# Performance work log

Measured on AMD Instinct MI355X. Metric: run time of the kernel, lower is better.

Reference implementation:

```python
import jax, jax.numpy as jnp
import numpy as np

N_NODES = 50000
N_EDGES = 800000
D = 128
L = 2

def mobius_add(x, y, c):
    xy = jnp.sum(x * y, axis=-1, keepdims=True)
    xx = jnp.sum(x * x, axis=-1, keepdims=True)
    yy = jnp.sum(y * y, axis=-1, keepdims=True)
    num = (1 + 2 * c * xy + c * yy) * x + (1 - c * xx) * y
    den = 1 + 2 * c * xy + c * c * xx * yy
    return num / den

def exp_map(x, v, c):
    vn = jnp.linalg.norm(v, axis=-1, keepdims=True)
    sc = jnp.sqrt(c)
    second = jnp.tanh(sc * vn / 2) * v / (sc * vn)
    return mobius_add(x, second, c)

def log_map(x, y, c):
    a = mobius_add(-x, y, c)
    an = jnp.linalg.norm(a, axis=-1, keepdims=True)
    sc = jnp.sqrt(c)
    return 2 / sc * jnp.arctanh(sc * an) * a / an

def l2norm(x, eps=1e-12):
    n = jnp.linalg.norm(x, axis=-1, keepdims=True)
    return x / jnp.maximum(n, eps)

def mean_agg(h, src, dst, n):
    # DGL update_all(copy_u('h','m'), mean('m','neigh')): mean over incoming edges
    s = jax.ops.segment_sum(h[src], dst, num_segments=n)  # [N, D]
    deg = jax.ops.segment_sum(jnp.ones((src.shape[0], 1), h.dtype), dst, num_segments=n)
    return s / jnp.maximum(deg, 1.0)

def setup_inputs() -> dict:
    key = jax.random.key(0)
    ks = jax.random.split(key, 12)
    w_scale = 1.0 / np.sqrt(D)
    return {
        'src': jax.random.randint(ks[0], (N_EDGES,), 0, N_NODES, dtype=jnp.int32),
        'dst': jax.random.randint(ks[1], (N_EDGES,), 0, N_NODES, dtype=jnp.int32),
        'e_emb': jax.random.normal(ks[2], (N_NODES, D), jnp.float32),
        # hyperbolic embeddings must lie well inside the Poincare ball
        'b_emb': jax.random.normal(ks[3], (N_NODES, D), jnp.float32) * 0.004,
        's_emb': jax.random.normal(ks[4], (N_NODES, D), jnp.float32),
        'e_W': jax.random.normal(ks[5], (L, D, D), jnp.float32) * w_scale,
        'e_b': jax.random.normal(ks[6], (L, D), jnp.float32) * 0.01,
        'b_W': jax.random.normal(ks[7], (L, D, D), jnp.float32) * w_scale,
        'b_b': jax.random.normal(ks[8], (L, D), jnp.float32) * 0.01,
        's_W': jax.random.normal(ks[9], (L, D, D), jnp.float32) * w_scale,
        's_b': jax.random.normal(ks[10], (L, D), jnp.float32) * 0.01,
        'b_curv': jnp.ones((1,), jnp.float32),
        's_curv': jnp.ones((1,), jnp.float32),
    }

def reference(src, dst, e_emb, b_emb, s_emb, e_W, e_b, b_W, b_b, s_W, s_b, b_curv, s_curv):
    n = e_emb.shape[0]
    bc = b_curv[0]
    sc = s_curv[0]
    for l in range(L):
        # euclidean: linear -> mean-aggregate -> LeakyReLU(0.2)
        e_h = e_emb @ e_W[l].T + e_b[l]
        e_new = mean_agg(e_h, src, dst, n)
        # hyperbolic: log-map to tangent at origin -> linear -> mean -> exp-map
        origin = jnp.zeros((1, D), b_emb.dtype)
        tang = log_map(origin, b_emb, bc)
        b_h = tang @ b_W[l].T + b_b[l]
        b_agg = mean_agg(b_h, src, dst, n)
        b_new = exp_map(origin, b_agg, bc)
        # spherical: normalize -> linear -> normalize -> mean -> normalize
        s_h = l2norm(s_emb)
        s_h = l2norm(s_h @ s_W[l].T + s_b[l])
        s_new = l2norm(mean_agg(s_h, src, dst, n))
        e_emb = jax.nn.leaky_relu(e_new, 0.2)
        b_emb = b_new
        s_emb = s_new
    return jnp.concatenate([e_emb, b_emb, s_emb], axis=1)  # [N, 3*D]
```

## Files before the change

### kernel.cpp

```cpp
#include <hip/hip_runtime.h>
#include <hip/hip_bf16.h>

#define NN 50000
#define NE 800000
#define DD 128

typedef unsigned int u32;
typedef __attribute__((ext_vector_type(8))) short short8;
typedef __attribute__((ext_vector_type(4))) float f32x4;
typedef __attribute__((ext_vector_type(2))) float f32x2;
typedef __attribute__((ext_vector_type(4))) u32 u32x4;

__device__ __forceinline__ u32 f2bf2(float a, float b){
  union { __hip_bfloat162 h; u32 u; } cv;
  cv.h = __float22bfloat162_rn(make_float2(a, b));
  return cv.u;
}
__device__ __forceinline__ f32x2 up2(u32 v){
  f32x2 r;
  r.x = __uint_as_float(v << 16);
  r.y = __uint_as_float(v & 0xffff0000u);
  return r;
}

struct InitArgs { const float* W[6]; u32* out; const int* dst; int* cnt; int* rank; };
__global__ __launch_bounds__(256) void k_init(InitArgs ia){
  const int bx = blockIdx.x;
  if (bx < 48){
    int tid = bx*256 + threadIdx.x;
    int mat = tid >> 11, rem = tid & 2047;
    int frag = rem >> 6, lane = rem & 63;
    int ct = frag >> 2, ks = frag & 3, rr = lane & 15, quad = lane >> 4;
    const float* p = ia.W[mat] + (ct*16 + rr)*128 + ks*32 + quad*8;
    float4 f0 = *(const float4*)p;
    float4 f1 = *(const float4*)(p + 4);
    u32x4 q;
    q.x = f2bf2(f0.x, f0.y); q.y = f2bf2(f0.z, f0.w);
    q.z = f2bf2(f1.x, f1.y); q.w = f2bf2(f1.z, f1.w);
    *(u32x4*)(ia.out + (size_t)tid*4) = q;
  } else {
    int i = (bx - 48)*256 + threadIdx.x;
    if (i < NE){
      int d = ia.dst[i];
      ia.rank[i] = atomicAdd(&ia.cnt[d], 1);
    }
  }
}

__global__ __launch_bounds__(256) void k_alloc(const int* __restrict__ cnt,
                                               int* __restrict__ row_beg,
                                               int* __restrict__ gcount){
  int i = blockIdx.x*256 + threadIdx.x;
  int lane = threadIdx.x & 63;
  int pc = (i < NN) ? ((cnt[i] + 1) & ~1) : 0;
  int incl = pc;
  #pragma unroll
  for (int off = 1; off < 64; off <<= 1){
    int u = __shfl_up(incl, off, 64);
    if (lane >= off) incl += u;
  }
  int wtot = __shfl(incl, 63, 64);
  int base = 0;
  if (lane == 0) base = atomicAdd(gcount, wtot);
  base = __shfl(base, 0, 64);
  int excl = base + incl - pc;
  if (i < NN) row_beg[i] = excl;
}

struct MainArgs {
  const float* A[3];
  const float* Bias[3];
  const u32* Wf;
  u32* H;
  const float* curv;
  const int* src;
  const int* dst;
  const int* rank;
  const int* row_beg;
  int* esrc;
};

#define GEMM_BLKS 471

__global__ __launch_bounds__(256,3) void k_main(MainArgs ma){
  const int bx = blockIdx.x;
  if (bx >= GEMM_BLKS){
    int i = (bx - GEMM_BLKS)*256 + threadIdx.x;
    if (i < NE){
      int d = ma.dst[i];
      ma.esrc[ma.row_beg[d] + ma.rank[i]] = (ma.src[i] + 1) * 192;
    }
    return;
  }
  const int m  = bx / 157;
  const int gx = bx % 157;
  const float* __restrict__ A    = ma.A[m];
  const float* __restrict__ Bias = ma.Bias[m];
  u32* __restrict__ H = ma.H;
  const int t = threadIdx.x;
  const int lane = t & 63;
  const int rr = lane & 15, quad = lane >> 4;

  __shared__ u32 Wlds[8192];
  {
    const u32x4* wsrc = (const u32x4*)(ma.Wf + (size_t)m*8192);
    #pragma unroll
    for (int it = 0; it < 8; ++it){
      int idx = it*256 + t;
      *(u32x4*)&Wlds[idx*4] = wsrc[idx];
    }
  }
  __syncthreads();

  float sc = 1.f;
  if (m == 1) sc = sqrtf(*ma.curv);

  const int nw = 157*4;
  for (int g = gx*4 + (t >> 6); g < 3125; g += nw){
    const float* ap = A + (size_t)(g*16 + rr)*DD + quad*8;
    float4 c[8];
    #pragma unroll
    for (int ks = 0; ks < 4; ++ks){
      c[2*ks]   = *(const float4*)(ap + ks*32);
      c[2*ks+1] = *(const float4*)(ap + ks*32 + 4);
    }
    if (m != 0){
      float p = 0.f;
      #pragma unroll
      for (int i = 0; i < 8; ++i)
        p += c[i].x*c[i].x + c[i].y*c[i].y + c[i].z*c[i].z + c[i].w*c[i].w;
      p += __shfl_xor(p, 16, 64);
      p += __shfl_xor(p, 32, 64);
      float nrm = sqrtf(p);
      float sca;
      if (m == 1){
        float x = sc * nrm;
        sca = (nrm > 1e-30f) ? (logf((1.f + x)/(1.f - x)) / (sc * nrm)) : 2.f;
      } else {
        sca = 1.f / fmaxf(nrm, 1e-12f);
      }
      #pragma unroll
      for (int i = 0; i < 8; ++i){ c[i].x*=sca; c[i].y*=sca; c[i].z*=sca; c[i].w*=sca; }
    }
    f32x4 acc[8];
    #pragma unroll
    for (int ct = 0; ct < 8; ++ct){ f32x4 z = {0.f,0.f,0.f,0.f}; acc[ct] = z; }
    #pragma unroll
    for (int ks = 0; ks < 4; ++ks){
      u32x4 bq;
      bq.x = f2bf2(c[2*ks].x,   c[2*ks].y);
      bq.y = f2bf2(c[2*ks].z,   c[2*ks].w);
      bq.z = f2bf2(c[2*ks+1].x, c[2*ks+1].y);
      bq.w = f2bf2(c[2*ks+1].z, c[2*ks+1].w);
      short8 bf = __builtin_bit_cast(short8, bq);
      #pragma unroll
      for (int ct = 0; ct < 8; ++ct){
        short8 wf = *(const short8*)&Wlds[((ct*4 + ks)*64 + lane)*4];
        acc[ct] = __builtin_amdgcn_mfma_f32_16x16x32_bf16(wf, bf, acc[ct], 0, 0, 0);
      }
    }
    #pragma unroll
    for (int ct = 0; ct < 8; ++ct){
      float4 bv = *(const float4*)(Bias + ct*16 + quad*4);
      acc[ct].x += bv.x; acc[ct].y += bv.y; acc[ct].z += bv.z; acc[ct].w += bv.w;
    }
    if (m == 2){
      float p = 0.f;
      #pragma unroll
      for (int ct = 0; ct < 8; ++ct)
        p += acc[ct].x*acc[ct].x + acc[ct].y*acc[ct].y + acc[ct].z*acc[ct].z + acc[ct].w*acc[ct].w;
      p += __shfl_xor(p, 16, 64);
      p += __shfl_xor(p, 32, 64);
      float inv = 1.f / fmaxf(sqrtf(p), 1e-12f);
      #pragma unroll
      for (int ct = 0; ct < 8; ++ct){ acc[ct].x*=inv; acc[ct].y*=inv; acc[ct].z*=inv; acc[ct].w*=inv; }
    }
    u32* hp = H + (size_t)(g*16 + rr + 1)*192 + m*64 + quad*2;
    #pragma unroll
    for (int ct = 0; ct < 8; ++ct){
      uint2 pk;
      pk.x = f2bf2(acc[ct].x, acc[ct].y);
      pk.y = f2bf2(acc[ct].z, acc[ct].w);
      *(uint2*)(hp + ct*8) = pk;
    }
  }
}

struct FusedArgs {
  const u32* H0;
  u32* H1;
  const int* row_beg;
  const int* cnt;
  const int* esrc;
  const u32* Wf;
  const float* Bias[3];
};

#define NSTR 388

__global__ __launch_bounds__(256,4) void k_fused(FusedArgs fa){
  const int t = threadIdx.x;
  const int w = t >> 6;
  const int lane = t & 63;
  const int half = lane >> 5, hl = lane & 31;
  const int rr = lane & 15, quad = lane >> 4;
  const int nbase = blockIdx.x * 16;

  __shared__ float S[16*NSTR];

  for (int i = 0; i < 4; ++i){
    const int nb = w*4 + i;
    const int node = nbase + nb;
    const int deg = fa.cnt[node];
    const int e0 = fa.row_beg[node];
    const int e1 = e0 + ((deg + 1) & ~1);
    const int* __restrict__ esrc = fa.esrc;
    const u32* __restrict__ Hf = fa.H0 + hl*2;

    f32x2 z2 = {0.f, 0.f};
    f32x2 a0[2] = {z2, z2};
    f32x2 a1[2] = {z2, z2};
    f32x2 a2[2] = {z2, z2};

    for (int base = e0; base < e1; base += 64){
      int nn = e1 - base; if (nn > 64) nn = 64;
      int sv = esrc[min(base + lane, e1 - 1)];
      int np = nn >> 1;
      int p = 0;
      for (; p + 4 <= np; p += 4){
        uint2 q[4][3];
        #pragma unroll
        for (int u = 0; u < 4; ++u){
          int soff = __shfl(sv, 2*(p + u) + half, 64);
          const u32* hp = Hf + soff;
          q[u][0] = *(const uint2*)hp;
          q[u][1] = *(const uint2*)(hp + 64);
          q[u][2] = *(const uint2*)(hp + 128);
        }
        #pragma unroll
        for (int u = 0; u < 4; ++u){
          a0[0] += up2(q[u][0].x); a0[1] += up2(q[u][0].y);
          a1[0] += up2(q[u][1].x); a1[1] += up2(q[u][1].y);
          a2[0] += up2(q[u][2].x); a2[1] += up2(q[u][2].y);
        }
      }
      for (; p < np; ++p){
        int soff = __shfl(sv, 2*p + half, 64);
        const u32* hp = Hf + soff;
        uint2 q0 = *(const uint2*)hp;
        uint2 q1 = *(const uint2*)(hp + 64);
        uint2 q2 = *(const uint2*)(hp + 128);
        a0[0] += up2(q0.x); a0[1] += up2(q0.y);
        a1[0] += up2(q1.x); a1[1] += up2(q1.y);
        a2[0] += up2(q2.x); a2[1] += up2(q2.y);
      }
    }

    #pragma unroll
    for (int j = 0; j < 2; ++j){
      a0[j].x += __shfl_xor(a0[j].x, 32, 64); a0[j].y += __shfl_xor(a0[j].y, 32, 64);
      a1[j].x += __shfl_xor(a1[j].x, 32, 64); a1[j].y += __shfl_xor(a1[j].y, 32, 64);
      a2[j].x += __shfl_xor(a2[j].x, 32, 64); a2[j].y += __shfl_xor(a2[j].y, 32, 64);
    }
    float inv = 1.f / (float)max(deg, 1);
    #pragma unroll
    for (int j = 0; j < 2; ++j){ a0[j] *= inv; a1[j] *= inv; a2[j] *= inv; }

    float p2 = a2[0].x*a2[0].x + a2[0].y*a2[0].y + a2[1].x*a2[1].x + a2[1].y*a2[1].y;
    #pragma unroll
    for (int off = 1; off < 32; off <<= 1) p2 += __shfl_xor(p2, off, 64);
    float s2 = 1.f / fmaxf(sqrtf(p2), 1e-12f);

    float* sp = &S[nb*NSTR];
    if (half == 0){
      f32x4 v0 = { a0[0].x > 0.f ? a0[0].x : 0.2f*a0[0].x,
                   a0[0].y > 0.f ? a0[0].y : 0.2f*a0[0].y,
                   a0[1].x > 0.f ? a0[1].x : 0.2f*a0[1].x,
                   a0[1].y > 0.f ? a0[1].y : 0.2f*a0[1].y };
      *(f32x4*)(sp + hl*4) = v0;
      f32x4 v1 = { a1[0].x, a1[0].y, a1[1].x, a1[1].y };
      *(f32x4*)(sp + 128 + hl*4) = v1;
    } else {
      f32x4 v2 = { a2[0].x*s2, a2[0].y*s2, a2[1].x*s2, a2[1].y*s2 };
      *(f32x4*)(sp + 256 + hl*4) = v2;
    }
  }
  __syncthreads();

  if (w < 3){
    const int m = w;
    short8 bf[4];
    const float* sp = &S[rr*NSTR + m*128];
    #pragma unroll
    for (int ks = 0; ks < 4; ++ks){
      f32x4 lo = *(const f32x4*)(sp + ks*32 + quad*8);
      f32x4 hi = *(const f32x4*)(sp + ks*32 + quad*8 + 4);
      u32x4 bq;
      bq.x = f2bf2(lo.x, lo.y); bq.y = f2bf2(lo.z, lo.w);
      bq.z = f2bf2(hi.x, hi.y); bq.w = f2bf2(hi.z, hi.w);
      bf[ks] = __builtin_bit_cast(short8, bq);
    }
    const u32* __restrict__ wbase = fa.Wf + (size_t)m*8192;
    const float* __restrict__ Bias = fa.Bias[m];
    f32x4 acc[8];
    #pragma unroll
    for (int ct = 0; ct < 8; ++ct){ f32x4 z = {0.f,0.f,0.f,0.f}; acc[ct] = z; }
    #pragma unroll
    for (int ct = 0; ct < 8; ++ct){
      short8 wfr[4];
      #pragma unroll
      for (int ks = 0; ks < 4; ++ks)
        wfr[ks] = *(const short8*)(wbase + ((ct*4 + ks)*64 + lane)*4);
      #pragma unroll
      for (int ks = 0; ks < 4; ++ks)
        acc[ct] = __builtin_amdgcn_mfma_f32_16x16x32_bf16(wfr[ks], bf[ks], acc[ct], 0, 0, 0);
    }
    #pragma unroll
    for (int ct = 0; ct < 8; ++ct){
      float4 bv = *(const float4*)(Bias + ct*16 + quad*4);
      acc[ct].x += bv.x; acc[ct].y += bv.y; acc[ct].z += bv.z; acc[ct].w += bv.w;
    }
    if (m == 2){
      float p = 0.f;
      #pragma unroll
      for (int ct = 0; ct < 8; ++ct)
        p += acc[ct].x*acc[ct].x + acc[ct].y*acc[ct].y + acc[ct].z*acc[ct].z + acc[ct].w*acc[ct].w;
      p += __shfl_xor(p, 16, 64);
      p += __shfl_xor(p, 32, 64);
      float nv = 1.f / fmaxf(sqrtf(p), 1e-12f);
      #pragma unroll
      for (int ct = 0; ct < 8; ++ct){ acc[ct].x*=nv; acc[ct].y*=nv; acc[ct].z*=nv; acc[ct].w*=nv; }
    }
    u32* hp = fa.H1 + (size_t)(nbase + rr + 1)*192 + m*64 + quad*2;
    #pragma unroll
    for (int ct = 0; ct < 8; ++ct){
      uint2 pk;
      pk.x = f2bf2(acc[ct].x, acc[ct].y);
      pk.y = f2bf2(acc[ct].z, acc[ct].w);
      *(uint2*)(hp + ct*8) = pk;
    }
  }
}

struct AggArgs {
  const u32* H;
  float* O;
  const int* row_beg;
  const int* cnt;
  const int* esrc;
  const float* curv;
};

__global__ __launch_bounds__(256) void k_agg(AggArgs aa){
  const int tid = threadIdx.x;
  const int lane = tid & 63;
  const int half = lane >> 5, hl = lane & 31;
  const int node = blockIdx.x*4 + (tid >> 6);
  if (node >= NN) return;
  const int deg = aa.cnt[node];
  const int e0 = aa.row_beg[node];
  const int e1 = e0 + ((deg + 1) & ~1);
  const int* __restrict__ esrc = aa.esrc;
  const u32* __restrict__ Hf = aa.H + hl*2;

  f32x2 z2 = {0.f, 0.f};
  f32x2 a0[2] = {z2, z2};
  f32x2 a1[2] = {z2, z2};
  f32x2 a2[2] = {z2, z2};

  for (int base = e0; base < e1; base += 64){
    int nn = e1 - base; if (nn > 64) nn = 64;
    int sv = esrc[min(base + lane, e1 - 1)];
    int np = nn >> 1;
    int p = 0;
    for (; p + 4 <= np; p += 4){
      uint2 q[4][3];
      #pragma unroll
      for (int u = 0; u < 4; ++u){
        int soff = __shfl(sv, 2*(p + u) + half, 64);
        const u32* hp = Hf + soff;
        q[u][0] = *(const uint2*)hp;
        q[u][1] = *(const uint2*)(hp + 64);
        q[u][2] = *(const uint2*)(hp + 128);
      }
      #pragma unroll
      for (int u = 0; u < 4; ++u){
        a0[0] += up2(q[u][0].x); a0[1] += up2(q[u][0].y);
        a1[0] += up2(q[u][1].x); a1[1] += up2(q[u][1].y);
        a2[0] += up2(q[u][2].x); a2[1] += up2(q[u][2].y);
      }
    }
    for (; p < np; ++p){
      int soff = __shfl(sv, 2*p + half, 64);
      const u32* hp = Hf + soff;
      uint2 q0 = *(const uint2*)hp;
      uint2 q1 = *(const uint2*)(hp + 64);
      uint2 q2 = *(const uint2*)(hp + 128);
      a0[0] += up2(q0.x); a0[1] += up2(q0.y);
      a1[0] += up2(q1.x); a1[1] += up2(q1.y);
      a2[0] += up2(q2.x); a2[1] += up2(q2.y);
    }
  }

  #pragma unroll
  for (int j = 0; j < 2; ++j){
    a0[j].x += __shfl_xor(a0[j].x, 32, 64); a0[j].y += __shfl_xor(a0[j].y, 32, 64);
    a1[j].x += __shfl_xor(a1[j].x, 32, 64); a1[j].y += __shfl_xor(a1[j].y, 32, 64);
    a2[j].x += __shfl_xor(a2[j].x, 32, 64); a2[j].y += __shfl_xor(a2[j].y, 32, 64);
  }
  float inv = 1.f / (float)max(deg, 1);
  #pragma unroll
  for (int j = 0; j < 2; ++j){ a0[j] *= inv; a1[j] *= inv; a2[j] *= inv; }

  float p1 = a1[0].x*a1[0].x + a1[0].y*a1[0].y + a1[1].x*a1[1].x + a1[1].y*a1[1].y;
  float p2 = a2[0].x*a2[0].x + a2[0].y*a2[0].y + a2[1].x*a2[1].x + a2[1].y*a2[1].y;
  #pragma unroll
  for (int off = 1; off < 32; off <<= 1){
    p1 += __shfl_xor(p1, off, 64);
    p2 += __shfl_xor(p2, off, 64);
  }
  float n1 = sqrtf(p1);
  float scv = sqrtf(*aa.curv);
  float x = scv * n1;
  float s1 = (n1 > 1e-30f) ? (tanhf(0.5f*x) / x) : 0.5f;
  float s2 = 1.f / fmaxf(sqrtf(p2), 1e-12f);

  float* op = aa.O + (size_t)node*384;
  if (half == 0){
    float4 e4 = make_float4(a0[0].x > 0.f ? a0[0].x : 0.2f*a0[0].x,
                            a0[0].y > 0.f ? a0[0].y : 0.2f*a0[0].y,
                            a0[1].x > 0.f ? a0[1].x : 0.2f*a0[1].x,
                            a0[1].y > 0.f ? a0[1].y : 0.2f*a0[1].y);
    *(float4*)(op + hl*4) = e4;
    *(float4*)(op + 128 + hl*4) = make_float4(a1[0].x*s1, a1[0].y*s1, a1[1].x*s1, a1[1].y*s1);
  } else {
    *(float4*)(op + 256 + hl*4) = make_float4(a2[0].x*s2, a2[0].y*s2, a2[1].x*s2, a2[1].y*s2);
  }
}

extern "C" void kernel_launch(void* const* d_in, const int* in_sizes, int n_in,
                              void* d_out, int out_size, void* d_ws, size_t ws_size,
                              hipStream_t stream){
  (void)in_sizes; (void)n_in; (void)out_size; (void)ws_size;
  const int*   src    = (const int*)  d_in[0];
  const int*   dst    = (const int*)  d_in[1];
  const float* e_emb  = (const float*)d_in[2];
  const float* b_emb  = (const float*)d_in[3];
  const float* s_emb  = (const float*)d_in[4];
  const float* e_W    = (const float*)d_in[5];
  const float* e_b    = (const float*)d_in[6];
  const float* b_W    = (const float*)d_in[7];
  const float* b_b    = (const float*)d_in[8];
  const float* s_W    = (const float*)d_in[9];
  const float* s_b    = (const float*)d_in[10];
  const float* b_curv = (const float*)d_in[11];
  float* out = (float*)d_out;

  char* ws = (char*)d_ws;
  size_t off = 0;
  auto alloc = [&](size_t bytes) -> void* {
    void* p = (void*)(ws + off);
    off += (bytes + 255) & ~(size_t)255;
    return p;
  };
  int* cnt       = (int*)alloc((size_t)NN*4);
  int* row_beg   = (int*)alloc((size_t)NN*4);
  int* rank      = (int*)alloc((size_t)NE*4);
  int* gcount    = (int*)alloc(256);
  int* esrc      = (int*)alloc((size_t)(NE + NN + 64)*4);
  u32* h0        = (u32*)alloc((size_t)(NN+1)*192*4);
  u32* h1        = (u32*)alloc((size_t)(NN+1)*192*4);
  u32* wf        = (u32*)alloc((size_t)6*2048*16);

  (void)hipMemsetAsync(cnt, 0, (size_t)NN*4, stream);
  (void)hipMemsetAsync(gcount, 0, 4, stream);
  (void)hipMemsetAsync(esrc, 0, (size_t)(NE + NN + 64)*4, stream);
  (void)hipMemsetAsync(h0, 0, 768, stream);
  (void)hipMemsetAsync(h1, 0, 768, stream);

  InitArgs ia;
  ia.W[0] = e_W;          ia.W[1] = b_W;          ia.W[2] = s_W;
  ia.W[3] = e_W + 16384;  ia.W[4] = b_W + 16384;  ia.W[5] = s_W + 16384;
  ia.out = wf; ia.dst = dst; ia.cnt = cnt; ia.rank = rank;
  k_init<<<48 + (NE+255)/256, 256, 0, stream>>>(ia);

  k_alloc<<<(NN+255)/256, 256, 0, stream>>>(cnt, row_beg, gcount);

  MainArgs m;
  m.A[0]=e_emb; m.A[1]=b_emb; m.A[2]=s_emb;
  m.Bias[0]=e_b; m.Bias[1]=b_b; m.Bias[2]=s_b;
  m.Wf = wf; m.H = h0; m.curv = b_curv;
  m.src = src; m.dst = dst; m.rank = rank; m.row_beg = row_beg; m.esrc = esrc;
  k_main<<<GEMM_BLKS + (NE+255)/256, 256, 0, stream>>>(m);

  FusedArgs f;
  f.H0 = h0; f.H1 = h1;
  f.row_beg = row_beg; f.cnt = cnt; f.esrc = esrc;
  f.Wf = wf + 3*8192;
  f.Bias[0] = e_b + DD; f.Bias[1] = b_b + DD; f.Bias[2] = s_b + DD;
  k_fused<<<NN/16, 256, 0, stream>>>(f);

  AggArgs a;
  a.H = h1; a.O = out; a.row_beg = row_beg; a.cnt = cnt; a.esrc = esrc; a.curv = b_curv;
  k_agg<<<(NN + 3)/4, 256, 0, stream>>>(a);
}
```

Baseline: 433.9 us.

## Replace memsets with a prep kernel and split the GEMM to overlap CSR build

```diff
diff --git a/kernel.cpp b/kernel.cpp
--- a/kernel.cpp
+++ b/kernel.cpp
@@ -4,6 +4,7 @@
 #define NN 50000
 #define NE 800000
 #define DD 128
+#define GHALF 1563
 
 typedef unsigned int u32;
 typedef __attribute__((ext_vector_type(8))) short short8;
@@ -23,36 +24,33 @@
   return r;
 }
 
-struct InitArgs { const float* W[6]; u32* out; const int* dst; int* cnt; int* rank; };
-__global__ __launch_bounds__(256) void k_init(InitArgs ia){
-  const int bx = blockIdx.x;
-  if (bx < 48){
-    int tid = bx*256 + threadIdx.x;
-    int mat = tid >> 11, rem = tid & 2047;
-    int frag = rem >> 6, lane = rem & 63;
-    int ct = frag >> 2, ks = frag & 3, rr = lane & 15, quad = lane >> 4;
-    const float* p = ia.W[mat] + (ct*16 + rr)*128 + ks*32 + quad*8;
-    float4 f0 = *(const float4*)p;
-    float4 f1 = *(const float4*)(p + 4);
-    u32x4 q;
-    q.x = f2bf2(f0.x, f0.y); q.y = f2bf2(f0.z, f0.w);
-    q.z = f2bf2(f1.x, f1.y); q.w = f2bf2(f1.z, f1.w);
-    *(u32x4*)(ia.out + (size_t)tid*4) = q;
-  } else {
-    int i = (bx - 48)*256 + threadIdx.x;
-    if (i < NE){
-      int d = ia.dst[i];
-      ia.rank[i] = atomicAdd(&ia.cnt[d], 1);
-    }
-  }
+struct PrepArgs { const float* W[6]; u32* out; int* cnt; int* gcount; u32* h0; u32* h1; };
+__global__ __launch_bounds__(256) void k_prep(PrepArgs pa){
+  int tid = blockIdx.x*256 + threadIdx.x;
+  for (int i = tid; i < NN; i += 48*256) pa.cnt[i] = 0;
+  if (tid == 0) *pa.gcount = 0;
+  if (tid < 192) pa.h0[tid] = 0;
+  else if (tid < 384) pa.h1[tid - 192] = 0;
+  int mat = tid >> 11, rem = tid & 2047;
+  int frag = rem >> 6, lane = rem & 63;
+  int ct = frag >> 2, ks = frag & 3, rr = lane & 15, quad = lane >> 4;
+  const float* p = pa.W[mat] + (ct*16 + rr)*128 + ks*32 + quad*8;
+  float4 f0 = *(const float4*)p;
+  float4 f1 = *(const float4*)(p + 4);
+  u32x4 q;
+  q.x = f2bf2(f0.x, f0.y); q.y = f2bf2(f0.z, f0.w);
+  q.z = f2bf2(f1.x, f1.y); q.w = f2bf2(f1.z, f1.w);
+  *(u32x4*)(pa.out + (size_t)tid*4) = q;
 }
 
 __global__ __launch_bounds__(256) void k_alloc(const int* __restrict__ cnt,
                                                int* __restrict__ row_beg,
-                                               int* __restrict__ gcount){
+                                               int* __restrict__ gcount,
+                                               int* __restrict__ esrc){
   int i = blockIdx.x*256 + threadIdx.x;
   int lane = threadIdx.x & 63;
-  int pc = (i < NN) ? ((cnt[i] + 1) & ~1) : 0;
+  int deg = (i < NN) ? cnt[i] : 0;
+  int pc = (deg + 1) & ~1;
   int incl = pc;
   #pragma unroll
   for (int off = 1; off < 64; off <<= 1){
@@ -64,7 +62,10 @@
   if (lane == 0) base = atomicAdd(gcount, wtot);
   base = __shfl(base, 0, 64);
   int excl = base + incl - pc;
-  if (i < NN) row_beg[i] = excl;
+  if (i < NN){
+    row_beg[i] = excl;
+    if (deg & 1) esrc[excl + deg] = 0;
+  }
 }
 
 struct MainArgs {
@@ -75,20 +76,26 @@
   const float* curv;
   const int* src;
   const int* dst;
-  const int* rank;
+  int* rank;
   const int* row_beg;
+  int* cnt;
   int* esrc;
 };
 
 #define GEMM_BLKS 471
 
+template<int PHASE>
 __global__ __launch_bounds__(256,3) void k_main(MainArgs ma){
   const int bx = blockIdx.x;
   if (bx >= GEMM_BLKS){
     int i = (bx - GEMM_BLKS)*256 + threadIdx.x;
     if (i < NE){
       int d = ma.dst[i];
-      ma.esrc[ma.row_beg[d] + ma.rank[i]] = (ma.src[i] + 1) * 192;
+      if (PHASE == 0){
+        ma.rank[i] = atomicAdd(&ma.cnt[d], 1);
+      } else {
+        ma.esrc[ma.row_beg[d] + ma.rank[i]] = (ma.src[i] + 1) * 192;
+      }
     }
     return;
   }
@@ -115,8 +122,10 @@
   float sc = 1.f;
   if (m == 1) sc = sqrtf(*ma.curv);
 
+  const int glo = (PHASE == 0) ? 0 : GHALF;
+  const int ghi = (PHASE == 0) ? GHALF : 3125;
   const int nw = 157*4;
-  for (int g = gx*4 + (t >> 6); g < 3125; g += nw){
+  for (int g = glo + gx*4 + (t >> 6); g < ghi; g += nw){
     const float* ap = A + (size_t)(g*16 + rr)*DD + quad*8;
     float4 c[8];
     #pragma unroll
@@ -472,26 +481,26 @@
   u32* h1        = (u32*)alloc((size_t)(NN+1)*192*4);
   u32* wf        = (u32*)alloc((size_t)6*2048*16);
 
-  (void)hipMemsetAsync(cnt, 0, (size_t)NN*4, stream);
-  (void)hipMemsetAsync(gcount, 0, 4, stream);
-  (void)hipMemsetAsync(esrc, 0, (size_t)(NE + NN + 64)*4, stream);
-  (void)hipMemsetAsync(h0, 0, 768, stream);
-  (void)hipMemsetAsync(h1, 0, 768, stream);
-
-  InitArgs ia;
-  ia.W[0] = e_W;          ia.W[1] = b_W;          ia.W[2] = s_W;
-  ia.W[3] = e_W + 16384;  ia.W[4] = b_W + 16384;  ia.W[5] = s_W + 16384;
-  ia.out = wf; ia.dst = dst; ia.cnt = cnt; ia.rank = rank;
-  k_init<<<48 + (NE+255)/256, 256, 0, stream>>>(ia);
-
-  k_alloc<<<(NN+255)/256, 256, 0, stream>>>(cnt, row_beg, gcount);
+  PrepArgs pp;
+  pp.W[0] = e_W;          pp.W[1] = b_W;          pp.W[2] = s_W;
+  pp.W[3] = e_W + 16384;  pp.W[4] = b_W + 16384;  pp.W[5] = s_W + 16384;
+  pp.out = wf; pp.cnt = cnt; pp.gcount = gcount; pp.h0 = h0; pp.h1 = h1;
+  k_prep<<<48, 256, 0, stream>>>(pp);
 
   MainArgs m;
   m.A[0]=e_emb; m.A[1]=b_emb; m.A[2]=s_emb;
   m.Bias[0]=e_b; m.Bias[1]=b_b; m.Bias[2]=s_b;
   m.Wf = wf; m.H = h0; m.curv = b_curv;
-  m.src = src; m.dst = dst; m.rank = rank; m.row_beg = row_beg; m.esrc = esrc;
-  k_main<<<GEMM_BLKS + (NE+255)/256, 256, 0, stream>>>(m);
+  m.src = src; m.dst = dst; m.rank = rank; m.row_beg = row_beg;
+  m.cnt = cnt; m.esrc = esrc;
+
+  const int side_blks = (NE + 255)/256;
+
+  k_main<0><<<GEMM_BLKS + side_blks, 256, 0, stream>>>(m);
+
+  k_alloc<<<(NN+255)/256, 256, 0, stream>>>(cnt, row_beg, gcount, esrc);
+
+  k_main<1><<<GEMM_BLKS + side_blks, 256, 0, stream>>>(m);
 
   FusedArgs f;
   f.H0 = h0; f.H1 = h1;
```

Result: faster. 417.6 us (-3.7%).
